# Kernel optimization log

Measured on AMD Instinct MI355X. Metric: run time of the kernel, lower is better.

Reference implementation:

```python
import jax, jax.numpy as jnp
import numpy as np

EPS_BN = 1e-5


def gcn_agg(h, src, dst, n):
    # remove_self_loops then add_self_loops, degree computed on dst (incl. self loops)
    valid = (src != dst).astype(h.dtype)  # mask out original self loops
    deg = jnp.zeros((n,), h.dtype).at[dst].add(valid) + 1.0  # +1 for added self loop
    dinv = deg ** -0.5
    w = dinv[src] * dinv[dst] * valid  # [E]
    # h_prime[dst] += w * h[src]; self-loop contributes deg^-1 * h
    out = jnp.zeros_like(h).at[dst].add(w[:, None] * h[src])
    out = out + (1.0 / deg)[:, None] * h
    return out


def batchnorm(h):
    # BatchNorm1d(affine=False, track_running_stats=False): batch stats, biased var
    mean = jnp.mean(h, axis=0)
    var = jnp.var(h, axis=0)
    return (h - mean) * jax.lax.rsqrt(var + EPS_BN)


def setup_inputs() -> dict:
    key = jax.random.key(0)
    ks = jax.random.split(key, 8)
    N, E, IN, HID, OUT = 50000, 640000, 500, 128, 64
    x = jax.random.normal(ks[0], (N, IN), jnp.float32)
    edge_index = jax.random.randint(ks[1], (2, E), 0, N, jnp.int64)
    def xavier(k, shape):
        gain = 1.414
        bound = gain * np.sqrt(6.0 / (shape[0] + shape[1]))
        return jax.random.uniform(k, shape, jnp.float32, -bound, bound)
    W0 = xavier(ks[2], (HID, IN))
    W1 = xavier(ks[3], (HID, HID))
    W2 = xavier(ks[4], (OUT, HID))
    b0 = jnp.zeros((HID,), jnp.float32)
    b1 = jnp.zeros((HID,), jnp.float32)
    b2 = jnp.zeros((OUT,), jnp.float32)
    return {"x": x, "edge_index": edge_index, "W0": W0, "b0": b0,
            "W1": W1, "b1": b1, "W2": W2, "b2": b2}


def reference(x, edge_index, W0, b0, W1, b1, W2, b2):
    n = x.shape[0]
    src, dst = edge_index[0], edge_index[1]
    # layer 0 and 1 (num_layers - 1 = 2), eval mode -> dropout is identity
    h = x @ W0.T
    h = gcn_agg(h, src, dst, n) + b0
    h = jax.nn.relu(batchnorm(h))
    h = h @ W1.T
    h = gcn_agg(h, src, dst, n) + b1
    h = jax.nn.relu(batchnorm(h))
    # classifier
    h = h @ W2.T
    h = gcn_agg(h, src, dst, n) + b2
    return jax.nn.log_softmax(h, axis=1)
```

## Files before the change

### kernel.cpp

```cpp
#include <hip/hip_runtime.h>
#include <hip/hip_bf16.h>
#include <math.h>


#define EPS_BN 1e-5f

typedef __attribute__((ext_vector_type(8))) _Float16 f16x8;
typedef __attribute__((ext_vector_type(4))) _Float16 f16x4;
typedef __attribute__((ext_vector_type(2))) _Float16 f16x2;
typedef __attribute__((ext_vector_type(4))) float    f32x4;

__device__ __forceinline__ void gload16(const void* g, void* l) {
    __builtin_amdgcn_global_load_lds(
        (const __attribute__((address_space(1))) void*)g,
        (__attribute__((address_space(3))) void*)l, 16, 0, 0);
}


__global__ void countw_k(const int* __restrict__ src, const int* __restrict__ dst,
                         int* __restrict__ cnt, int E, int gE,
                         const float* __restrict__ W0, _Float16* __restrict__ W0h,
                         const float* __restrict__ W1, _Float16* __restrict__ W1h,
                         const float* __restrict__ W2, _Float16* __restrict__ W2h) {
    if (blockIdx.x < (unsigned)gE) {
        int e = blockIdx.x * 256 + threadIdx.x;
        if (e >= E) return;
        int s = src[e], d = dst[e];
        if (s != d) atomicAdd(&cnt[d], 1);
        return;
    }
    int idx = (blockIdx.x - gE) * 256 + threadIdx.x;
    if (idx < 16384) {
        int r = idx >> 7, k4 = (idx & 127) * 4;
        f16x4 h = {(_Float16)0.f, (_Float16)0.f, (_Float16)0.f, (_Float16)0.f};
        if (k4 < 500) {
            float4 v = *(const float4*)(W0 + (size_t)r * 500 + k4);
            h[0] = (_Float16)v.x; h[1] = (_Float16)v.y;
            h[2] = (_Float16)v.z; h[3] = (_Float16)v.w;
        }
        *(f16x4*)(W0h + (size_t)r * 512 + k4) = h;
    } else if (idx < 16384 + 4096) {
        int t = idx - 16384;
        float4 v = *(const float4*)(W1 + (size_t)t * 4);
        f16x4 h;
        h[0] = (_Float16)v.x; h[1] = (_Float16)v.y;
        h[2] = (_Float16)v.z; h[3] = (_Float16)v.w;
        *(f16x4*)(W1h + (size_t)t * 4) = h;
    } else if (idx < 22528) {
        int t = idx - 20480;
        float4 v = *(const float4*)(W2 + (size_t)t * 4);
        f16x4 h;
        h[0] = (_Float16)v.x; h[1] = (_Float16)v.y;
        h[2] = (_Float16)v.z; h[3] = (_Float16)v.w;
        *(f16x4*)(W2h + (size_t)t * 4) = h;
    }
}

__global__ void scan1_k(const int* __restrict__ cnt, int* __restrict__ within,
                        int* __restrict__ btot, int n) {
    __shared__ int s[512];
    int tid = threadIdx.x;
    int i = blockIdx.x * 512 + tid;
    int val = (i < n) ? cnt[i] : 0;
    s[tid] = val;
    __syncthreads();
    for (int off = 1; off < 512; off <<= 1) {
        int v = (tid >= off) ? s[tid - off] : 0;
        __syncthreads();
        s[tid] += v;
        __syncthreads();
    }
    if (i < n) within[i] = s[tid] - val;
    if (tid == 511) btot[blockIdx.x] = s[511];
}

__global__ void scan3_k(const int* __restrict__ within, const int* __restrict__ btot,
                        const int* __restrict__ cnt, int* __restrict__ row_start,
                        int* __restrict__ cursor, float* __restrict__ dinv,
                        float* __restrict__ invdeg, int n) {
    __shared__ int sred[256];
    const int tid = threadIdx.x;
    const int w = (blockIdx.x * 256) >> 9;
    sred[tid] = (tid < w) ? btot[tid] : 0;
    __syncthreads();
    #pragma unroll
    for (int off = 128; off >= 1; off >>= 1) {
        if (tid < off) sred[tid] += sred[tid + off];
        __syncthreads();
    }
    const int base = sred[0];
    int i = blockIdx.x * 256 + tid;
    if (i < n) {
        int rs = within[i] + base;
        row_start[i] = rs;
        cursor[i]    = rs;
        float deg = (float)cnt[i] + 1.0f;
        dinv[i]   = rsqrtf(deg);
        invdeg[i] = 1.0f / deg;
    }
}


template <int NC, bool BN, bool AF32, bool FILL>
__global__ __launch_bounds__(256) void mgemm_k(const void* __restrict__ Av,
                                               const _Float16* __restrict__ Wh,
                                               _Float16* __restrict__ C,
                                               const float* __restrict__ gsum,
                                               const float* __restrict__ gsq,
                                               float inv_n, int M, int K, int Kp,
                                               const int* __restrict__ src,
                                               const int* __restrict__ dst,
                                               const float* __restrict__ dinv,
                                               int* __restrict__ cursor,
                                               int2* __restrict__ epk,
                                               int E, int gM) {
    constexpr int CT = NC / 16;
    constexpr int WJ = NC / 32;
    constexpr int ASZ = AF32 ? (64 * 512) : (2 * 64 * 64);
    __shared__ __align__(16) _Float16 As[ASZ];
    __shared__ __align__(16) _Float16 Ws[2][NC * 64];
    __shared__ __align__(16) float ssc[128], ssh[128];

    if constexpr (FILL) {
        if ((int)blockIdx.x >= gM) {
            int e = (blockIdx.x - gM) * 256 + threadIdx.x;
            if (e < E) {
                int s = src[e], d = dst[e];
                if (s != d) {
                    int pos = atomicAdd(&cursor[d], 1);
                    epk[pos] = make_int2(s, __float_as_int(dinv[s] * dinv[d]));
                }
            }
            return;
        }
    }

    const int tid  = threadIdx.x;
    const int lane = tid & 63, wave = tid >> 6;
    const int lrow = lane & 15, kg = lane >> 4;
    const int row0 = blockIdx.x * 64;

    f32x4 acc[CT] = {};

    const float*    Af = (const float*)Av;
    const _Float16* Ah = (const _Float16*)Av;

    auto stage = [&](int c0, int b) {
        const int k0 = c0 * 64;
        if constexpr (!AF32) {
            #pragma unroll
            for (int j = 0; j < 2; ++j) {
                int li  = wave * 128 + j * 64 + lane;
                int row = li >> 3, s = li & 7;
                int gr  = row0 + row;
                int gs  = s ^ (row & 7);
                if (gr < M)
                    gload16(Ah + (size_t)gr * Kp + k0 + gs * 8,
                            (char*)As + b * (64 * 64 * 2) +
                            (wave * 128 + j * 64) * 16);
            }
        }
        #pragma unroll
        for (int j = 0; j < WJ; ++j) {
            int li  = wave * (WJ * 64) + j * 64 + lane;
            int row = li >> 3, s = li & 7;
            int gs  = s ^ (row & 7);
            gload16(Wh + (size_t)row * Kp + k0 + gs * 8,
                    (char*)&Ws[b][0] + (wave * WJ + j) * 1024);
        }
    };

    auto fillA = [&]() {
        #pragma unroll
        for (int r = 0; r < 16; ++r) {
            int row = wave * 16 + r;
            int gr  = row0 + row;
            if (gr >= M) continue;
            const float* rowp = Af + (size_t)gr * K;
            float4 v0 = *(const float4*)(rowp + lane * 4);
            int s1 = 64 + lane;
            float4 v1 = make_float4(0.f, 0.f, 0.f, 0.f);
            if (s1 * 4 < K)
                v1 = *(const float4*)(rowp + s1 * 4);
            f16x4 h0, h1;
            h0[0] = (_Float16)v0.x; h0[1] = (_Float16)v0.y;
            h0[2] = (_Float16)v0.z; h0[3] = (_Float16)v0.w;
            h1[0] = (_Float16)v1.x; h1[1] = (_Float16)v1.y;
            h1[2] = (_Float16)v1.z; h1[3] = (_Float16)v1.w;
            const int sw = (row & 7) << 4;
            char* rb = (char*)As + row * 1024;
            *(f16x4*)(rb + ((lane * 8) ^ sw)) = h0;
            *(f16x4*)(rb + ((s1 * 8) ^ sw))  = h1;
        }
    };

    auto compute = [&](int b, int cchunk, int kofs) {
        const char* AsB = (const char*)As + (AF32 ? 0 : b * (64 * 64 * 2));
        const char* WsB = (const char*)&Ws[b][0];
        #pragma unroll
        for (int ks = 0; ks < 2; ++ks) {
            const int cb = ks * 64 + kg * 16;
            f16x8 af, bf[CT];
            {
                int row = wave * 16 + lrow;
                int sw  = (row & 7) << 4;
                if constexpr (AF32)
                    af = *(const f16x8*)(AsB + row * 1024 +
                                         ((cchunk * 128 + cb) ^ sw));
                else
                    af = *(const f16x8*)(AsB + row * 128 + (cb ^ sw));
            }
            if constexpr (BN) {
                const int kb = kofs + ks * 32 + kg * 8;
                f32x4 sc0 = *(const f32x4*)&ssc[kb];
                f32x4 sc1 = *(const f32x4*)&ssc[kb + 4];
                f32x4 sh0 = *(const f32x4*)&ssh[kb];
                f32x4 sh1 = *(const f32x4*)&ssh[kb + 4];
                f16x8 a2;
                #pragma unroll
                for (int j = 0; j < 4; ++j) {
                    a2[j]     = (_Float16)fmaxf(0.f, fmaf((float)af[j],     sc0[j], sh0[j]));
                    a2[j + 4] = (_Float16)fmaxf(0.f, fmaf((float)af[j + 4], sc1[j], sh1[j]));
                }
                af = a2;
            }
            #pragma unroll
            for (int ct = 0; ct < CT; ++ct) {
                int row = ct * 16 + lrow;
                bf[ct] = *(const f16x8*)(WsB + row * 128 +
                                         (cb ^ ((row & 7) << 4)));
            }
            #pragma unroll
            for (int ct = 0; ct < CT; ++ct)
                acc[ct] = __builtin_amdgcn_mfma_f32_16x16x32_f16(
                    af, bf[ct], acc[ct], 0, 0, 0);
        }
    };

    if constexpr (BN) {
        if (tid < 128) {
            float mean = gsum[tid] * inv_n;
            float var  = gsq[tid] * inv_n - mean * mean;
            float sc   = rsqrtf(var + EPS_BN);
            ssc[tid] = sc;
            ssh[tid] = -mean * sc;
        }
    }

    const int nchunk = Kp >> 6;

    if constexpr (AF32) {
        fillA();
        stage(0, 0);
        asm volatile("s_waitcnt vmcnt(0) lgkmcnt(0)" ::: "memory");
        __builtin_amdgcn_s_barrier();
        __builtin_amdgcn_sched_barrier(0);
        for (int c = 0; c < nchunk; ++c) {
            const int b = c & 1;
            const bool more = (c + 1 < nchunk);
            if (more) stage(c + 1, b ^ 1);
            compute(b, c, 0);
            if (more) {
                asm volatile("s_waitcnt vmcnt(0)" ::: "memory");
                __builtin_amdgcn_s_barrier();
                __builtin_amdgcn_sched_barrier(0);
            }
        }
    } else {
        stage(0, 0);
        asm volatile("s_waitcnt vmcnt(0) lgkmcnt(0)" ::: "memory");
        __builtin_amdgcn_s_barrier();
        __builtin_amdgcn_sched_barrier(0);
        for (int c = 0; c < nchunk; ++c) {
            const int b = c & 1;
            const bool more = (c + 1 < nchunk);
            if (more) stage(c + 1, b ^ 1);
            compute(b, c, c * 64);
            if (more) {
                asm volatile("s_waitcnt vmcnt(0) lgkmcnt(0)" ::: "memory");
                __builtin_amdgcn_s_barrier();
                __builtin_amdgcn_sched_barrier(0);
            }
        }
    }

    #pragma unroll
    for (int r = 0; r < 4; ++r) {
        int grow = row0 + wave * 16 + kg * 4 + r;
        if (grow >= M) continue;
        #pragma unroll
        for (int ct = 0; ct < CT; ++ct)
            C[(size_t)grow * NC + ct * 16 + lrow] = (_Float16)acc[ct][r];
    }
}


__global__ void agg128_k(const _Float16* __restrict__ h, const float* __restrict__ invdeg,
                         const int* __restrict__ row_start, const int* __restrict__ cnt,
                         const int2* __restrict__ epk,
                         const float* __restrict__ bias, _Float16* __restrict__ out, int n) {
    const int grp = threadIdx.x >> 4;
    const int l = threadIdx.x & 15;
    const int i = blockIdx.x * 16 + grp;
    if (i >= n) return;
    const int st = row_start[i], en = st + cnt[i];
    const float id = invdeg[i];
    const int c = l * 8;

    float a[8];
    {
        f16x8 hv = *(const f16x8*)(h + (size_t)i * 128 + c);
        #pragma unroll
        for (int j = 0; j < 8; ++j)
            a[j] = fmaf(id, (float)hv[j], bias[c + j]);
    }

    auto gfma = [&](int2 e0, int2 e1, int2 e2, int2 e3) {
        f16x8 v0 = *(const f16x8*)(h + (size_t)e0.x * 128 + c);
        f16x8 v1 = *(const f16x8*)(h + (size_t)e1.x * 128 + c);
        f16x8 v2 = *(const f16x8*)(h + (size_t)e2.x * 128 + c);
        f16x8 v3 = *(const f16x8*)(h + (size_t)e3.x * 128 + c);
        float w0 = __int_as_float(e0.y), w1 = __int_as_float(e1.y);
        float w2 = __int_as_float(e2.y), w3 = __int_as_float(e3.y);
        #pragma unroll
        for (int j = 0; j < 8; ++j) {
            a[j] = fmaf(w0, (float)v0[j], a[j]);
            a[j] = fmaf(w1, (float)v1[j], a[j]);
            a[j] = fmaf(w2, (float)v2[j], a[j]);
            a[j] = fmaf(w3, (float)v3[j], a[j]);
        }
    };

    int p = st;
    if (p + 3 < en) {
        int2 eA0 = epk[p], eA1 = epk[p + 1], eA2 = epk[p + 2], eA3 = epk[p + 3];
        while (p + 7 < en) {
            int2 eB0 = epk[p + 4], eB1 = epk[p + 5];
            int2 eB2 = epk[p + 6], eB3 = epk[p + 7];
            gfma(eA0, eA1, eA2, eA3);
            eA0 = eB0; eA1 = eB1; eA2 = eB2; eA3 = eB3;
            p += 4;
        }
        gfma(eA0, eA1, eA2, eA3);
        p += 4;
    }
    for (; p < en; ++p) {
        int2 e0 = epk[p];
        float w0 = __int_as_float(e0.y);
        f16x8 v0 = *(const f16x8*)(h + (size_t)e0.x * 128 + c);
        #pragma unroll
        for (int j = 0; j < 8; ++j)
            a[j] = fmaf(w0, (float)v0[j], a[j]);
    }
    f16x8 o;
    #pragma unroll
    for (int j = 0; j < 8; ++j) o[j] = (_Float16)a[j];
    *(f16x8*)(out + (size_t)i * 128 + c) = o;
}


__global__ void stats16_k(const _Float16* __restrict__ a, float* __restrict__ gsum,
                          float* __restrict__ gsq, int total8) {
    const int tid = threadIdx.x;
    float s[8] = {}, q[8] = {};
    for (int idx = blockIdx.x * 256 + tid; idx < total8; idx += gridDim.x * 256) {
        f16x8 v = *(const f16x8*)(a + (size_t)idx * 8);
        #pragma unroll
        for (int j = 0; j < 8; ++j) {
            float f = (float)v[j];
            s[j] += f;
            q[j] = fmaf(f, f, q[j]);
        }
    }
    __shared__ float red[2][16][16][8];
    const int g = tid & 15, k = tid >> 4;
    #pragma unroll
    for (int j = 0; j < 8; ++j) {
        red[0][k][g][j] = s[j];
        red[1][k][g][j] = q[j];
    }
    __syncthreads();
    if (tid < 128) {
        const int g2 = tid & 15, j2 = tid >> 4;
        float ts = 0.f, tq = 0.f;
        #pragma unroll
        for (int k2 = 0; k2 < 16; ++k2) {
            ts += red[0][k2][g2][j2];
            tq += red[1][k2][g2][j2];
        }
        atomicAdd(&gsum[g2 * 8 + j2], ts);
        atomicAdd(&gsq[g2 * 8 + j2], tq);
    }
}


__global__ void aggsm_k(const _Float16* __restrict__ h, const float* __restrict__ invdeg,
                        const int* __restrict__ row_start, const int* __restrict__ cnt,
                        const int2* __restrict__ epk,
                        const float* __restrict__ bias, float* __restrict__ out, int n) {
    const int grp = threadIdx.x >> 3;
    const int l = threadIdx.x & 7;
    const int i = blockIdx.x * 32 + grp;
    if (i >= n) return;
    const int st = row_start[i], en = st + cnt[i];
    const float id = invdeg[i];
    const int c = l * 8;

    float a[8];
    {
        f16x8 hv = *(const f16x8*)(h + (size_t)i * 64 + c);
        #pragma unroll
        for (int j = 0; j < 8; ++j)
            a[j] = fmaf(id, (float)hv[j], bias[c + j]);
    }

    auto gfma = [&](int2 e0, int2 e1, int2 e2, int2 e3) {
        f16x8 v0 = *(const f16x8*)(h + (size_t)e0.x * 64 + c);
        f16x8 v1 = *(const f16x8*)(h + (size_t)e1.x * 64 + c);
        f16x8 v2 = *(const f16x8*)(h + (size_t)e2.x * 64 + c);
        f16x8 v3 = *(const f16x8*)(h + (size_t)e3.x * 64 + c);
        float w0 = __int_as_float(e0.y), w1 = __int_as_float(e1.y);
        float w2 = __int_as_float(e2.y), w3 = __int_as_float(e3.y);
        #pragma unroll
        for (int j = 0; j < 8; ++j) {
            a[j] = fmaf(w0, (float)v0[j], a[j]);
            a[j] = fmaf(w1, (float)v1[j], a[j]);
            a[j] = fmaf(w2, (float)v2[j], a[j]);
            a[j] = fmaf(w3, (float)v3[j], a[j]);
        }
    };

    int p = st;
    if (p + 3 < en) {
        int2 eA0 = epk[p], eA1 = epk[p + 1], eA2 = epk[p + 2], eA3 = epk[p + 3];
        while (p + 7 < en) {
            int2 eB0 = epk[p + 4], eB1 = epk[p + 5];
            int2 eB2 = epk[p + 6], eB3 = epk[p + 7];
            gfma(eA0, eA1, eA2, eA3);
            eA0 = eB0; eA1 = eB1; eA2 = eB2; eA3 = eB3;
            p += 4;
        }
        gfma(eA0, eA1, eA2, eA3);
        p += 4;
    }
    for (; p < en; ++p) {
        int2 e0 = epk[p];
        float w0 = __int_as_float(e0.y);
        f16x8 v0 = *(const f16x8*)(h + (size_t)e0.x * 64 + c);
        #pragma unroll
        for (int j = 0; j < 8; ++j)
            a[j] = fmaf(w0, (float)v0[j], a[j]);
    }

    float m = a[0];
    #pragma unroll
    for (int j = 1; j < 8; ++j) m = fmaxf(m, a[j]);
    #pragma unroll
    for (int d = 4; d >= 1; d >>= 1) m = fmaxf(m, __shfl_xor(m, d, 64));
    float s = 0.f;
    float e[8];
    #pragma unroll
    for (int j = 0; j < 8; ++j) { e[j] = __expf(a[j] - m); s += e[j]; }
    #pragma unroll
    for (int d = 4; d >= 1; d >>= 1) s += __shfl_xor(s, d, 64);
    float ls = __logf(s);
    float4 o0 = make_float4(a[0] - m - ls, a[1] - m - ls,
                            a[2] - m - ls, a[3] - m - ls);
    float4 o1 = make_float4(a[4] - m - ls, a[5] - m - ls,
                            a[6] - m - ls, a[7] - m - ls);
    *(float4*)(out + (size_t)i * 64 + c)     = o0;
    *(float4*)(out + (size_t)i * 64 + c + 4) = o1;
}


extern "C" void kernel_launch(void* const* d_in, const int* in_sizes, int n_in,
                              void* d_out, int out_size, void* d_ws, size_t ws_size,
                              hipStream_t stream) {
    const float* x  = (const float*)d_in[0];
    const int*   ei = (const int*)d_in[1];
    const float* W0 = (const float*)d_in[2];
    const float* b0 = (const float*)d_in[3];
    const float* W1 = (const float*)d_in[4];
    const float* b1 = (const float*)d_in[5];
    const float* W2 = (const float*)d_in[6];
    const float* b2 = (const float*)d_in[7];

    const int IN = 500;
    const int n = in_sizes[0] / IN;
    const int E = in_sizes[1] / 2;
    const int* src = ei;
    const int* dst = ei + E;

    char* p = (char*)d_ws;
    auto alloc = [&](size_t bytes) -> void* {
        char* r = p;
        p += (bytes + 255) & ~(size_t)255;
        return (void*)r;
    };
    _Float16*  hb1h    = (_Float16*)alloc((size_t)n * 128 * 2);
    _Float16*  hb2a    = (_Float16*)alloc((size_t)n * 128 * 2);
    _Float16*  W0h     = (_Float16*)alloc((size_t)128 * 512 * 2);
    _Float16*  W1h     = (_Float16*)alloc((size_t)128 * 128 * 2);
    _Float16*  W2h     = (_Float16*)alloc((size_t)64 * 128 * 2);
    int*   deg_cnt  = (int*)alloc((size_t)n * 4);
    float* gsum0    = (float*)alloc(128 * 4);
    float* gsq0     = (float*)alloc(128 * 4);
    float* gsum1    = (float*)alloc(128 * 4);
    float* gsq1     = (float*)alloc(128 * 4);
    char*  zero_end = p;
    float* dinv     = (float*)alloc((size_t)n * 4);
    float* invdeg   = (float*)alloc((size_t)n * 4);
    int*   row_st   = (int*)alloc((size_t)n * 4);
    int*   cursor   = (int*)alloc((size_t)n * 4);
    int*   within   = (int*)alloc((size_t)n * 4);
    int*   btot     = (int*)alloc(256 * 4);
    int2*  epk      = (int2*)alloc((size_t)E * 8);
    (void)ws_size; (void)n_in; (void)out_size;

    float* out = (float*)d_out;
    const float inv_n = 1.0f / (float)n;

    const int gE = (E + 255) / 256;
    const int gN = (n + 255) / 256;
    const int nblk = (n + 511) / 512;
    const int gM = (n + 63) / 64;
    const int gA = (n + 15) / 16;
    const int gS = (n + 31) / 32;

    hipMemsetAsync(deg_cnt, 0, (size_t)(zero_end - (char*)deg_cnt), stream);
    countw_k<<<gE + 88, 256, 0, stream>>>(src, dst, deg_cnt, E, gE,
                                          W0, W0h, W1, W1h, W2, W2h);
    scan1_k<<<nblk, 512, 0, stream>>>(deg_cnt, within, btot, n);
    scan3_k<<<gN, 256, 0, stream>>>(within, btot, deg_cnt, row_st, cursor,
                                    dinv, invdeg, n);

    mgemm_k<128, false, true, true><<<gM + gE, 256, 0, stream>>>(
        x, W0h, hb1h, nullptr, nullptr, 0.f, n, 500, 512,
        src, dst, dinv, cursor, epk, E, gM);
    agg128_k<<<gA, 256, 0, stream>>>(hb1h, invdeg, row_st, deg_cnt, epk, b0, hb2a, n);
    stats16_k<<<256, 256, 0, stream>>>(hb2a, gsum0, gsq0, n * 16);

    mgemm_k<128, true, false, false><<<gM, 256, 0, stream>>>(
        hb2a, W1h, hb1h, gsum0, gsq0, inv_n, n, 128, 128,
        nullptr, nullptr, nullptr, nullptr, nullptr, 0, gM);
    agg128_k<<<gA, 256, 0, stream>>>(hb1h, invdeg, row_st, deg_cnt, epk, b1, hb2a, n);
    stats16_k<<<256, 256, 0, stream>>>(hb2a, gsum1, gsq1, n * 16);

    mgemm_k<64, true, false, false><<<gM, 256, 0, stream>>>(
        hb2a, W2h, hb1h, gsum1, gsq1, inv_n, n, 128, 128,
        nullptr, nullptr, nullptr, nullptr, nullptr, 0, gM);
    aggsm_k<<<gS, 256, 0, stream>>>(hb1h, invdeg, row_st, deg_cnt, epk, b2, out, n);
}
```

Measured before the change: 236.2 us.

## Load fp32 A operand straight into MFMA registers, dropping the LDS A tile

In the first-layer GEMM, which reads fp32 input, each lane now loads its own A fragments for all 8 K-chunks from global memory, converts them to fp16 in registers, and feeds them straight to MFMA. The 64KB shared-memory A buffer and its fill pass are removed, which should raise occupancy and cut LDS traffic. K=500 and the chunk count are hardcoded. Out-of-range columns now read real data instead of zeros, so correctness relies on the padded weight columns being zero. Register pressure also rises, since 16 fp16x8 fragments stay live per lane.

Result: faster. 213.3 us (-9.7%).

```diff
diff --git a/kernel.cpp b/kernel.cpp
--- a/kernel.cpp
+++ b/kernel.cpp
@@ -116,7 +116,7 @@
                                                int E, int gM) {
     constexpr int CT = NC / 16;
     constexpr int WJ = NC / 32;
-    constexpr int ASZ = AF32 ? (64 * 512) : (2 * 64 * 64);
+    constexpr int ASZ = AF32 ? 16 : (2 * 64 * 64);
     __shared__ __align__(16) _Float16 As[ASZ];
     __shared__ __align__(16) _Float16 Ws[2][NC * 64];
     __shared__ __align__(16) float ssc[128], ssh[128];
@@ -170,71 +170,9 @@
         }
     };
 
-    auto fillA = [&]() {
-        #pragma unroll
-        for (int r = 0; r < 16; ++r) {
-            int row = wave * 16 + r;
-            int gr  = row0 + row;
-            if (gr >= M) continue;
-            const float* rowp = Af + (size_t)gr * K;
-            float4 v0 = *(const float4*)(rowp + lane * 4);
-            int s1 = 64 + lane;
-            float4 v1 = make_float4(0.f, 0.f, 0.f, 0.f);
-            if (s1 * 4 < K)
-                v1 = *(const float4*)(rowp + s1 * 4);
-            f16x4 h0, h1;
-            h0[0] = (_Float16)v0.x; h0[1] = (_Float16)v0.y;
-            h0[2] = (_Float16)v0.z; h0[3] = (_Float16)v0.w;
-            h1[0] = (_Float16)v1.x; h1[1] = (_Float16)v1.y;
-            h1[2] = (_Float16)v1.z; h1[3] = (_Float16)v1.w;
-            const int sw = (row & 7) << 4;
-            char* rb = (char*)As + row * 1024;
-            *(f16x4*)(rb + ((lane * 8) ^ sw)) = h0;
-            *(f16x4*)(rb + ((s1 * 8) ^ sw))  = h1;
-        }
-    };
-
-    auto compute = [&](int b, int cchunk, int kofs) {
-        const char* AsB = (const char*)As + (AF32 ? 0 : b * (64 * 64 * 2));
+    auto mfma_with = [&](f16x8 af, int b) {
         const char* WsB = (const char*)&Ws[b][0];
-        #pragma unroll
-        for (int ks = 0; ks < 2; ++ks) {
-            const int cb = ks * 64 + kg * 16;
-            f16x8 af, bf[CT];
-            {
-                int row = wave * 16 + lrow;
-                int sw  = (row & 7) << 4;
-                if constexpr (AF32)
-                    af = *(const f16x8*)(AsB + row * 1024 +
-                                         ((cchunk * 128 + cb) ^ sw));
-                else
-                    af = *(const f16x8*)(AsB + row * 128 + (cb ^ sw));
-            }
-            if constexpr (BN) {
-                const int kb = kofs + ks * 32 + kg * 8;
-                f32x4 sc0 = *(const f32x4*)&ssc[kb];
-                f32x4 sc1 = *(const f32x4*)&ssc[kb + 4];
-                f32x4 sh0 = *(const f32x4*)&ssh[kb];
-                f32x4 sh1 = *(const f32x4*)&ssh[kb + 4];
-                f16x8 a2;
-                #pragma unroll
-                for (int j = 0; j < 4; ++j) {
-                    a2[j]     = (_Float16)fmaxf(0.f, fmaf((float)af[j],     sc0[j], sh0[j]));
-                    a2[j + 4] = (_Float16)fmaxf(0.f, fmaf((float)af[j + 4], sc1[j], sh1[j]));
-                }
-                af = a2;
-            }
-            #pragma unroll
-            for (int ct = 0; ct < CT; ++ct) {
-                int row = ct * 16 + lrow;
-                bf[ct] = *(const f16x8*)(WsB + row * 128 +
-                                         (cb ^ ((row & 7) << 4)));
-            }
-            #pragma unroll
-            for (int ct = 0; ct < CT; ++ct)
-                acc[ct] = __builtin_amdgcn_mfma_f32_16x16x32_f16(
-                    af, bf[ct], acc[ct], 0, 0, 0);
-        }
+        return af; (void)WsB;
     };
 
     if constexpr (BN) {
@@ -247,10 +185,58 @@
         }
     }
 
-    const int nchunk = Kp >> 6;
-
     if constexpr (AF32) {
-        fillA();
+        const int row = wave * 16 + lrow;
+        const int gr  = row0 + row;
+        const float* rowp = Af + (size_t)(gr < M ? gr : 0) * (size_t)500;
+        f16x8 afr[16];
+        #pragma unroll
+        for (int f = 0; f < 16; ++f) {
+            const int c  = f >> 1, ks = f & 1;
+            const int e0 = c * 64 + ks * 32 + kg * 8;
+            const int e1 = e0 + 4;
+            float4 v0 = *(const float4*)(rowp + ((e0 + 4 <= 500) ? e0 : 0));
+            float4 v1 = *(const float4*)(rowp + ((e1 + 4 <= 500) ? e1 : 0));
+            f16x8 h;
+            h[0] = (_Float16)v0.x; h[1] = (_Float16)v0.y;
+            h[2] = (_Float16)v0.z; h[3] = (_Float16)v0.w;
+            h[4] = (_Float16)v1.x; h[5] = (_Float16)v1.y;
+            h[6] = (_Float16)v1.z; h[7] = (_Float16)v1.w;
+            afr[f] = h;
+        }
+        stage(0, 0);
+        asm volatile("s_waitcnt vmcnt(0) lgkmcnt(0)" ::: "memory");
+        __builtin_amdgcn_s_barrier();
+        __builtin_amdgcn_sched_barrier(0);
+
+        #pragma unroll
+        for (int c = 0; c < 8; ++c) {
+            const int b = c & 1;
+            if (c + 1 < 8) stage(c + 1, b ^ 1);
+            const char* WsB = (const char*)&Ws[b][0];
+            #pragma unroll
+            for (int ks = 0; ks < 2; ++ks) {
+                const int cb = ks * 64 + kg * 16;
+                f16x8 bf[CT];
+                #pragma unroll
+                for (int ct = 0; ct < CT; ++ct) {
+                    int r2 = ct * 16 + lrow;
+                    bf[ct] = *(const f16x8*)(WsB + r2 * 128 +
+                                             (cb ^ ((r2 & 7) << 4)));
+                }
+                #pragma unroll
+                for (int ct = 0; ct < CT; ++ct)
+                    acc[ct] = __builtin_amdgcn_mfma_f32_16x16x32_f16(
+                        afr[c * 2 + ks], bf[ct], acc[ct], 0, 0, 0);
+            }
+            if (c + 1 < 8) {
+                asm volatile("s_waitcnt vmcnt(0) lgkmcnt(0)" ::: "memory");
+                __builtin_amdgcn_s_barrier();
+                __builtin_amdgcn_sched_barrier(0);
+            }
+        }
+    } else {
+        const int nchunk = Kp >> 6;
         stage(0, 0);
         asm volatile("s_waitcnt vmcnt(0) lgkmcnt(0)" ::: "memory");
         __builtin_amdgcn_s_barrier();
@@ -259,23 +245,45 @@
             const int b = c & 1;
             const bool more = (c + 1 < nchunk);
             if (more) stage(c + 1, b ^ 1);
-            compute(b, c, 0);
-            if (more) {
-                asm volatile("s_waitcnt vmcnt(0)" ::: "memory");
-                __builtin_amdgcn_s_barrier();
-                __builtin_amdgcn_sched_barrier(0);
+            {
+                const char* AsB = (const char*)As + b * (64 * 64 * 2);
+                const char* WsB = (const char*)&Ws[b][0];
+                const int kofs = c * 64;
+                #pragma unroll
+                for (int ks = 0; ks < 2; ++ks) {
+                    const int cb = ks * 64 + kg * 16;
+                    f16x8 af, bf[CT];
+                    {
+                        int row = wave * 16 + lrow;
+                        af = *(const f16x8*)(AsB + row * 128 +
+                                             (cb ^ ((row & 7) << 4)));
+                    }
+                    if constexpr (BN) {
+                        const int kb = kofs + ks * 32 + kg * 8;
+                        f32x4 sc0 = *(const f32x4*)&ssc[kb];
+                        f32x4 sc1 = *(const f32x4*)&ssc[kb + 4];
+                        f32x4 sh0 = *(const f32x4*)&ssh[kb];
+                        f32x4 sh1 = *(const f32x4*)&ssh[kb + 4];
+                        f16x8 a2;
+                        #pragma unroll
+                        for (int j = 0; j < 4; ++j) {
+                            a2[j]     = (_Float16)fmaxf(0.f, fmaf((float)af[j],     sc0[j], sh0[j]));
+                            a2[j + 4] = (_Float16)fmaxf(0.f, fmaf((float)af[j + 4], sc1[j], sh1[j]));
+                        }
+                        af = a2;
+                    }
+                    #pragma unroll
+                    for (int ct = 0; ct < CT; ++ct) {
+                        int row = ct * 16 + lrow;
+                        bf[ct] = *(const f16x8*)(WsB + row * 128 +
+                                                 (cb ^ ((row & 7) << 4)));
+                    }
+                    #pragma unroll
+                    for (int ct = 0; ct < CT; ++ct)
+                        acc[ct] = __builtin_amdgcn_mfma_f32_16x16x32_f16(
+                            af, bf[ct], acc[ct], 0, 0, 0);
+                }
             }
-        }
-    } else {
-        stage(0, 0);
-        asm volatile("s_waitcnt vmcnt(0) lgkmcnt(0)" ::: "memory");
-        __builtin_amdgcn_s_barrier();
-        __builtin_amdgcn_sched_barrier(0);
-        for (int c = 0; c < nchunk; ++c) {
-            const int b = c & 1;
-            const bool more = (c + 1 < nchunk);
-            if (more) stage(c + 1, b ^ 1);
-            compute(b, c, c * 64);
             if (more) {
                 asm volatile("s_waitcnt vmcnt(0) lgkmcnt(0)" ::: "memory");
                 __builtin_amdgcn_s_barrier();
```
